# Kernel tuning notes

Measured on AMD Instinct MI355X. Metric: run time of the kernel, lower is better.

The kernel has to match this reference:

```python
import jax, jax.numpy as jnp
import numpy as np

NEG_SLOPE = 0.2

def setup_inputs() -> dict:
    key = jax.random.key(0)
    ks = jax.random.split(key, 10)
    N, E, D = 50000, 1250000, 64
    indices = jax.random.randint(ks[0], (2, E), 0, N, dtype=jnp.int64)
    features = jax.random.normal(ks[1], (N, D), dtype=jnp.float32)
    edge_types = jax.random.randint(ks[2], (E,), 0, 4, dtype=jnp.int64)
    s = 1.0 / np.sqrt(D)
    return {
        "indices": indices,
        "features": features,
        "edge_types": edge_types,
        "num_nodes": N,
        "W1_w": jax.random.uniform(ks[3], (D, D), jnp.float32, -s, s),
        "W1_b": jax.random.uniform(ks[4], (D,), jnp.float32, -s, s),
        "W2_w": jax.random.uniform(ks[5], (D, D), jnp.float32, -s, s),
        "W2_b": jax.random.uniform(ks[6], (D,), jnp.float32, -s, s),
        "W_att_w": jax.random.uniform(ks[7], (D, D), jnp.float32, -s, s),
        "W_att_b": jax.random.uniform(ks[8], (D,), jnp.float32, -s, s),
        "a": jax.random.normal(ks[9], (2 * D, 1), jnp.float32) * np.sqrt(2.0 / (2 * D + 1)),
    }


def reference(indices, features, edge_types, num_nodes, W1_w, W1_b, W2_w, W2_b, W_att_w, W_att_b, a):
    src, dst = indices[0], indices[1]
    D = W_att_w.shape[0]
    scaling = 1.0 / jnp.sqrt(jnp.float32(D))

    # Attention transform; cat([h_src, h_dst]) @ a == h_src@a1 + h_dst@a2
    h_trans = features @ W_att_w.T + W_att_b              # (N, D)
    a1, a2 = a[:D, 0], a[D:, 0]
    s_src = h_trans @ a1                                  # (N,)
    s_dst = h_trans @ a2                                  # (N,)
    e_raw = s_src[src] + s_dst[dst]                       # (E,)

    bias = jnp.where(edge_types == 0, 5.0, 0.0)           # ingredient bias
    e = jax.nn.leaky_relu((e_raw + bias) * scaling, NEG_SLOPE).astype(jnp.float32)

    # segment softmax over destination nodes (max is detached in original)
    max_score = jax.lax.stop_gradient(jax.ops.segment_max(e, dst, num_segments=num_nodes))
    max_score = jnp.where(jnp.isfinite(max_score), max_score, -1e9)
    exp_e = jnp.exp(e - max_score[dst])                   # (E,)
    denom = jax.ops.segment_sum(exp_e, dst, num_segments=num_nodes)
    alpha = exp_e / (denom[dst] + 1e-9)                   # (E,)

    # message passing
    h_msg = features @ W1_w.T + W1_b                      # (N, D)
    weighted = h_msg[src] * alpha[:, None]                # (E, D)
    h_neigh = jax.ops.segment_sum(weighted, dst, num_segments=num_nodes)  # (N, D)

    h_self = features                                     # in_dim == out_dim
    sum_h = h_self + h_neigh
    prod_h = h_self * h_neigh
    h_out = jax.nn.leaky_relu(sum_h + prod_h @ W2_w.T + W2_b, NEG_SLOPE)
    return h_out
```

## Files before the change

### kernel.cpp

```cpp
#include <hip/hip_runtime.h>
#include <math.h>

#define DD 64
#define WSTR 68
#define NEG_SLOPE 0.2f
#define SCALING 0.125f
#define CAP 64

__device__ __forceinline__ float lrelu(float x) { return x >= 0.0f ? x : NEG_SLOPE * x; }

__device__ __forceinline__ unsigned bf16_rne(float f) {
    unsigned u = __float_as_uint(f);
    u += 0x7FFFu + ((u >> 16) & 1u);
    return u >> 16;
}

__device__ __forceinline__ float bfly_sum64(float v) {
    #pragma unroll
    for (int off = 1; off < 64; off <<= 1) v += __shfl_xor(v, off);
    return v;
}

__global__ void k_prep(const float* __restrict__ Watt, const float* __restrict__ Wattb,
                       const float* __restrict__ a, float* __restrict__ v12,
                       float* __restrict__ c12) {
    int k = threadIdx.x;
    float s1 = 0.f, s2 = 0.f;
    for (int d = 0; d < DD; ++d) {
        float w = Watt[d * DD + k];
        s1 = fmaf(w, a[d], s1);
        s2 = fmaf(w, a[DD + d], s2);
    }
    v12[k] = s1;
    v12[DD + k] = s2;
    float b = Wattb[k];
    float p1 = bfly_sum64(b * a[k]);
    float p2 = bfly_sum64(b * a[DD + k]);
    if (k == 0) { c12[0] = p1; c12[1] = p2; }
}

__global__ __launch_bounds__(256) void k_node1(
        const float* __restrict__ feat, const float* __restrict__ W1,
        const float* __restrict__ W1b, const float* __restrict__ v12,
        const float* __restrict__ c12,
        float* __restrict__ s_src, float* __restrict__ s_dst,
        unsigned short* __restrict__ hmsg16, int N) {
    __shared__ float W1p[DD * WSTR];
    __shared__ float fsh[4][4 * DD];
    int t = threadIdx.x;
    for (int i = t; i < DD * DD; i += 256) {
        int d = i >> 6, k = i & 63;
        W1p[d * WSTR + k] = W1[i];
    }
    __syncthreads();
    int lane = t & 63, wslot = t >> 6;
    float c1 = c12[0], c2 = c12[1];
    float v1l = v12[lane], v2l = v12[DD + lane];
    float b = W1b[lane];
    float* fs = fsh[wslot];
    int n0 = (blockIdx.x * 4 + wslot) * 4;
    if (n0 >= N) return;

    float fd[4], p1[4], p2[4];
    #pragma unroll
    for (int i = 0; i < 4; ++i) {
        int n = n0 + i;
        fd[i] = (n < N) ? feat[n * DD + lane] : 0.f;
        fs[i * DD + lane] = fd[i];
        p1[i] = fd[i] * v1l;
        p2[i] = fd[i] * v2l;
    }
    #pragma unroll
    for (int off = 1; off < 64; off <<= 1) {
        #pragma unroll
        for (int i = 0; i < 4; ++i) {
            p1[i] += __shfl_xor(p1[i], off);
            p2[i] += __shfl_xor(p2[i], off);
        }
    }
    float acc[4] = {b, b, b, b};
    const float4* wrow = (const float4*)&W1p[lane * WSTR];
    #pragma unroll
    for (int k4 = 0; k4 < 16; ++k4) {
        float4 w = wrow[k4];
        #pragma unroll
        for (int i = 0; i < 4; ++i) {
            float4 f = *(const float4*)&fs[i * DD + k4 * 4];
            acc[i] = fmaf(f.x, w.x, acc[i]);
            acc[i] = fmaf(f.y, w.y, acc[i]);
            acc[i] = fmaf(f.z, w.z, acc[i]);
            acc[i] = fmaf(f.w, w.w, acc[i]);
        }
    }
    #pragma unroll
    for (int i = 0; i < 4; ++i) {
        int n = n0 + i;
        if (n < N) {
            hmsg16[n * DD + lane] = (unsigned short)bf16_rne(acc[i]);
            if (lane == 0) { s_src[n] = p1[i] + c1; s_dst[n] = p2[i] + c2; }
        }
    }
}

__global__ void k_bucket(const int* __restrict__ src, const int* __restrict__ dst,
                         const int* __restrict__ et,
                         const float* __restrict__ s_src, const float* __restrict__ s_dst,
                         int* __restrict__ cnt, unsigned* __restrict__ wpack, int E) {
    int i = blockIdx.x * blockDim.x + threadIdx.x;
    if (i >= E) return;
    int d = dst[i], s = src[i];
    float e = s_src[s] + s_dst[d] + (et[i] == 0 ? 5.0f : 0.0f);
    float w = __expf(lrelu(e * SCALING));
    int slot = atomicAdd(&cnt[d], 1);
    if (slot > CAP - 1) slot = CAP - 1;
    wpack[(d << 6) + slot] = (bf16_rne(w) << 16) | (unsigned)s;
}

__global__ __launch_bounds__(256) void k_gather(
        const float* __restrict__ feat, const unsigned* __restrict__ hmsg,
        const float* __restrict__ W2, const float* __restrict__ W2b,
        const int* __restrict__ cnt, const unsigned* __restrict__ wpack,
        float* __restrict__ out, int N) {
    __shared__ float W2p[DD * WSTR];
    __shared__ float plds[4][DD];
    int t = threadIdx.x;
    for (int i = t; i < DD * DD; i += 256) {
        int d = i >> 6, k = i & 63;
        W2p[d * WSTR + k] = W2[i];
    }
    __syncthreads();
    int lane = t & 63, wslot = t >> 6;
    int c = lane & 31, h = lane >> 5;
    int n = (blockIdx.x * 256 + t) >> 6;
    if (n >= N) return;
    int m = cnt[n]; if (m > CAP) m = CAP;
    unsigned u = wpack[(n << 6) + lane];
    if (lane >= m) u = 0;

    float ax = 0.f, ay = 0.f, bx = 0.f, by = 0.f, l = 0.f;
    int tt = 0;
    for (; tt + 8 <= m; tt += 8) {
        unsigned e0 = __shfl(u, tt + h);
        unsigned e1 = __shfl(u, tt + 2 + h);
        unsigned e2 = __shfl(u, tt + 4 + h);
        unsigned e3 = __shfl(u, tt + 6 + h);
        unsigned v0 = hmsg[(e0 & 0xFFFFu) * 32 + c];
        unsigned v1 = hmsg[(e1 & 0xFFFFu) * 32 + c];
        unsigned v2 = hmsg[(e2 & 0xFFFFu) * 32 + c];
        unsigned v3 = hmsg[(e3 & 0xFFFFu) * 32 + c];
        float w0 = __uint_as_float(e0 & 0xFFFF0000u);
        float w1 = __uint_as_float(e1 & 0xFFFF0000u);
        float w2 = __uint_as_float(e2 & 0xFFFF0000u);
        float w3 = __uint_as_float(e3 & 0xFFFF0000u);
        ax = fmaf(w0, __uint_as_float(v0 << 16), ax);
        ay = fmaf(w0, __uint_as_float(v0 & 0xFFFF0000u), ay);
        bx = fmaf(w1, __uint_as_float(v1 << 16), bx);
        by = fmaf(w1, __uint_as_float(v1 & 0xFFFF0000u), by);
        ax = fmaf(w2, __uint_as_float(v2 << 16), ax);
        ay = fmaf(w2, __uint_as_float(v2 & 0xFFFF0000u), ay);
        bx = fmaf(w3, __uint_as_float(v3 << 16), bx);
        by = fmaf(w3, __uint_as_float(v3 & 0xFFFF0000u), by);
        l += (w0 + w1) + (w2 + w3);
    }
    for (; tt < m; tt += 2) {
        unsigned e0 = __shfl(u, tt + h);
        unsigned v0 = hmsg[(e0 & 0xFFFFu) * 32 + c];
        float w0 = __uint_as_float(e0 & 0xFFFF0000u);
        ax = fmaf(w0, __uint_as_float(v0 << 16), ax);
        ay = fmaf(w0, __uint_as_float(v0 & 0xFFFF0000u), ay);
        l += w0;
    }
    ax += bx; ay += by;
    ax += __shfl_xor(ax, 32);
    ay += __shfl_xor(ay, 32);
    l  += __shfl_xor(l, 32);
    float inv = 1.f / (l + 1e-9f);

    float* pl = plds[wslot];
    if (h == 0) { pl[2 * c] = ax * inv; pl[2 * c + 1] = ay * inv; }
    float hn = pl[lane];
    float fd = feat[n * DD + lane];
    pl[lane] = fd * hn;
    float acc2 = W2b[lane];
    const float4* wrow = (const float4*)&W2p[lane * WSTR];
    #pragma unroll
    for (int k4 = 0; k4 < 16; ++k4) {
        float4 w = wrow[k4];
        float4 pk = *(const float4*)&pl[k4 * 4];
        acc2 = fmaf(pk.x, w.x, acc2);
        acc2 = fmaf(pk.y, w.y, acc2);
        acc2 = fmaf(pk.z, w.z, acc2);
        acc2 = fmaf(pk.w, w.w, acc2);
    }
    out[n * DD + lane] = lrelu(fd + hn + acc2);
}

extern "C" void kernel_launch(void* const* d_in, const int* in_sizes, int n_in,
                              void* d_out, int out_size, void* d_ws, size_t ws_size,
                              hipStream_t stream) {
    const int*   indices = (const int*)d_in[0];
    const float* feat    = (const float*)d_in[1];
    const int*   etype   = (const int*)d_in[2];
    const float* W1      = (const float*)d_in[4];
    const float* W1b     = (const float*)d_in[5];
    const float* W2      = (const float*)d_in[6];
    const float* W2b     = (const float*)d_in[7];
    const float* Watt    = (const float*)d_in[8];
    const float* Wattb   = (const float*)d_in[9];
    const float* a       = (const float*)d_in[10];

    const int E = in_sizes[2];
    const int N = in_sizes[1] / DD;
    const int* src = indices;
    const int* dst = indices + E;

    float* ws = (float*)d_ws;
    float*    v12   = ws;
    float*    c12   = ws + 128;
    float*    s_src = ws + 192;
    float*    s_dst = s_src + N;
    int*      cnt   = (int*)(s_dst + N);
    unsigned* hmsg  = (unsigned*)(cnt + N);
    unsigned* wpack = hmsg + (size_t)N * 32;

    hipMemsetAsync(cnt, 0, (size_t)N * sizeof(int), stream);
    k_prep<<<1, 64, 0, stream>>>(Watt, Wattb, a, v12, c12);
    k_node1<<<(N + 15) / 16, 256, 0, stream>>>(feat, W1, W1b, v12, c12,
                                               s_src, s_dst, (unsigned short*)hmsg, N);
    k_bucket<<<(E + 255) / 256, 256, 0, stream>>>(src, dst, etype, s_src, s_dst,
                                                  cnt, wpack, E);
    k_gather<<<(N + 3) / 4, 256, 0, stream>>>(feat, hmsg, W2, W2b,
                                              cnt, wpack, (float*)d_out, N);
}
```

Baseline: 249.8 us.

## Apply W1 after aggregation, gather bf16 features, fold prep kernel, persistent gather

Uses linearity to aggregate weighted bf16 raw features per destination and apply W1 once per node afterwards, with the bias scaled by the weight sum. The separate prep kernel is removed: every node1 block recomputes the attention projection vectors itself, and node1 now only converts features to bf16. The gather kernel becomes a persistent grid-stride loop over 1024 blocks, amortising the load of both weight matrices into shared memory. The cost is a second 64x64 matvec per node in the gather and redundant per-block recomputation of the projection vectors.

```diff
diff --git a/kernel.cpp b/kernel.cpp
--- a/kernel.cpp
+++ b/kernel.cpp
@@ -21,43 +21,29 @@
     return v;
 }
 
-__global__ void k_prep(const float* __restrict__ Watt, const float* __restrict__ Wattb,
-                       const float* __restrict__ a, float* __restrict__ v12,
-                       float* __restrict__ c12) {
-    int k = threadIdx.x;
-    float s1 = 0.f, s2 = 0.f;
-    for (int d = 0; d < DD; ++d) {
-        float w = Watt[d * DD + k];
-        s1 = fmaf(w, a[d], s1);
-        s2 = fmaf(w, a[DD + d], s2);
-    }
-    v12[k] = s1;
-    v12[DD + k] = s2;
-    float b = Wattb[k];
-    float p1 = bfly_sum64(b * a[k]);
-    float p2 = bfly_sum64(b * a[DD + k]);
-    if (k == 0) { c12[0] = p1; c12[1] = p2; }
-}
-
 __global__ __launch_bounds__(256) void k_node1(
-        const float* __restrict__ feat, const float* __restrict__ W1,
-        const float* __restrict__ W1b, const float* __restrict__ v12,
-        const float* __restrict__ c12,
+        const float* __restrict__ feat, const float* __restrict__ Watt,
+        const float* __restrict__ Wattb, const float* __restrict__ a,
         float* __restrict__ s_src, float* __restrict__ s_dst,
-        unsigned short* __restrict__ hmsg16, int N) {
-    __shared__ float W1p[DD * WSTR];
-    __shared__ float fsh[4][4 * DD];
+        unsigned* __restrict__ feat16, int N) {
+    __shared__ float v1s[DD], v2s[DD], csh[2];
     int t = threadIdx.x;
-    for (int i = t; i < DD * DD; i += 256) {
-        int d = i >> 6, k = i & 63;
-        W1p[d * WSTR + k] = W1[i];
+    if (t < 64) {
+        float s1 = 0.f, s2 = 0.f;
+        for (int d = 0; d < DD; ++d) {
+            float w = Watt[d * DD + t];
+            s1 = fmaf(w, a[d], s1);
+            s2 = fmaf(w, a[DD + d], s2);
+        }
+        v1s[t] = s1; v2s[t] = s2;
+        float b = Wattb[t];
+        float p1 = bfly_sum64(b * a[t]);
+        float p2 = bfly_sum64(b * a[DD + t]);
+        if (t == 0) { csh[0] = p1; csh[1] = p2; }
     }
     __syncthreads();
     int lane = t & 63, wslot = t >> 6;
-    float c1 = c12[0], c2 = c12[1];
-    float v1l = v12[lane], v2l = v12[DD + lane];
-    float b = W1b[lane];
-    float* fs = fsh[wslot];
+    float v1l = v1s[lane], v2l = v2s[lane], c1 = csh[0], c2 = csh[1];
     int n0 = (blockIdx.x * 4 + wslot) * 4;
     if (n0 >= N) return;
 
@@ -66,7 +52,6 @@
     for (int i = 0; i < 4; ++i) {
         int n = n0 + i;
         fd[i] = (n < N) ? feat[n * DD + lane] : 0.f;
-        fs[i * DD + lane] = fd[i];
         p1[i] = fd[i] * v1l;
         p2[i] = fd[i] * v2l;
     }
@@ -78,25 +63,14 @@
             p2[i] += __shfl_xor(p2[i], off);
         }
     }
-    float acc[4] = {b, b, b, b};
-    const float4* wrow = (const float4*)&W1p[lane * WSTR];
-    #pragma unroll
-    for (int k4 = 0; k4 < 16; ++k4) {
-        float4 w = wrow[k4];
-        #pragma unroll
-        for (int i = 0; i < 4; ++i) {
-            float4 f = *(const float4*)&fs[i * DD + k4 * 4];
-            acc[i] = fmaf(f.x, w.x, acc[i]);
-            acc[i] = fmaf(f.y, w.y, acc[i]);
-            acc[i] = fmaf(f.z, w.z, acc[i]);
-            acc[i] = fmaf(f.w, w.w, acc[i]);
-        }
-    }
     #pragma unroll
     for (int i = 0; i < 4; ++i) {
         int n = n0 + i;
+        unsigned me = bf16_rne(fd[i]);
+        unsigned pair = me | (__shfl_down(me, 1) << 16);
+        unsigned v = __shfl(pair, 2 * lane);
         if (n < N) {
-            hmsg16[n * DD + lane] = (unsigned short)bf16_rne(acc[i]);
+            if (lane < 32) feat16[n * 32 + lane] = v;
             if (lane == 0) { s_src[n] = p1[i] + c1; s_dst[n] = p2[i] + c2; }
         }
     }
@@ -117,82 +91,98 @@
 }
 
 __global__ __launch_bounds__(256) void k_gather(
-        const float* __restrict__ feat, const unsigned* __restrict__ hmsg,
+        const float* __restrict__ feat, const unsigned* __restrict__ feat16,
+        const float* __restrict__ W1, const float* __restrict__ W1b,
         const float* __restrict__ W2, const float* __restrict__ W2b,
         const int* __restrict__ cnt, const unsigned* __restrict__ wpack,
         float* __restrict__ out, int N) {
-    __shared__ float W2p[DD * WSTR];
+    __shared__ float W1p[DD * WSTR], W2p[DD * WSTR];
     __shared__ float plds[4][DD];
     int t = threadIdx.x;
     for (int i = t; i < DD * DD; i += 256) {
         int d = i >> 6, k = i & 63;
+        W1p[d * WSTR + k] = W1[i];
         W2p[d * WSTR + k] = W2[i];
     }
     __syncthreads();
     int lane = t & 63, wslot = t >> 6;
     int c = lane & 31, h = lane >> 5;
-    int n = (blockIdx.x * 256 + t) >> 6;
-    if (n >= N) return;
-    int m = cnt[n]; if (m > CAP) m = CAP;
-    unsigned u = wpack[(n << 6) + lane];
-    if (lane >= m) u = 0;
-
-    float ax = 0.f, ay = 0.f, bx = 0.f, by = 0.f, l = 0.f;
-    int tt = 0;
-    for (; tt + 8 <= m; tt += 8) {
-        unsigned e0 = __shfl(u, tt + h);
-        unsigned e1 = __shfl(u, tt + 2 + h);
-        unsigned e2 = __shfl(u, tt + 4 + h);
-        unsigned e3 = __shfl(u, tt + 6 + h);
-        unsigned v0 = hmsg[(e0 & 0xFFFFu) * 32 + c];
-        unsigned v1 = hmsg[(e1 & 0xFFFFu) * 32 + c];
-        unsigned v2 = hmsg[(e2 & 0xFFFFu) * 32 + c];
-        unsigned v3 = hmsg[(e3 & 0xFFFFu) * 32 + c];
-        float w0 = __uint_as_float(e0 & 0xFFFF0000u);
-        float w1 = __uint_as_float(e1 & 0xFFFF0000u);
-        float w2 = __uint_as_float(e2 & 0xFFFF0000u);
-        float w3 = __uint_as_float(e3 & 0xFFFF0000u);
-        ax = fmaf(w0, __uint_as_float(v0 << 16), ax);
-        ay = fmaf(w0, __uint_as_float(v0 & 0xFFFF0000u), ay);
-        bx = fmaf(w1, __uint_as_float(v1 << 16), bx);
-        by = fmaf(w1, __uint_as_float(v1 & 0xFFFF0000u), by);
-        ax = fmaf(w2, __uint_as_float(v2 << 16), ax);
-        ay = fmaf(w2, __uint_as_float(v2 & 0xFFFF0000u), ay);
-        bx = fmaf(w3, __uint_as_float(v3 << 16), bx);
-        by = fmaf(w3, __uint_as_float(v3 & 0xFFFF0000u), by);
-        l += (w0 + w1) + (w2 + w3);
-    }
-    for (; tt < m; tt += 2) {
-        unsigned e0 = __shfl(u, tt + h);
-        unsigned v0 = hmsg[(e0 & 0xFFFFu) * 32 + c];
-        float w0 = __uint_as_float(e0 & 0xFFFF0000u);
-        ax = fmaf(w0, __uint_as_float(v0 << 16), ax);
-        ay = fmaf(w0, __uint_as_float(v0 & 0xFFFF0000u), ay);
-        l += w0;
-    }
-    ax += bx; ay += by;
-    ax += __shfl_xor(ax, 32);
-    ay += __shfl_xor(ay, 32);
-    l  += __shfl_xor(l, 32);
-    float inv = 1.f / (l + 1e-9f);
-
+    float b1l = W1b[lane], b2l = W2b[lane];
+    const float4* wrow1 = (const float4*)&W1p[lane * WSTR];
+    const float4* wrow2 = (const float4*)&W2p[lane * WSTR];
     float* pl = plds[wslot];
-    if (h == 0) { pl[2 * c] = ax * inv; pl[2 * c + 1] = ay * inv; }
-    float hn = pl[lane];
-    float fd = feat[n * DD + lane];
-    pl[lane] = fd * hn;
-    float acc2 = W2b[lane];
-    const float4* wrow = (const float4*)&W2p[lane * WSTR];
-    #pragma unroll
-    for (int k4 = 0; k4 < 16; ++k4) {
-        float4 w = wrow[k4];
-        float4 pk = *(const float4*)&pl[k4 * 4];
-        acc2 = fmaf(pk.x, w.x, acc2);
-        acc2 = fmaf(pk.y, w.y, acc2);
-        acc2 = fmaf(pk.z, w.z, acc2);
-        acc2 = fmaf(pk.w, w.w, acc2);
-    }
-    out[n * DD + lane] = lrelu(fd + hn + acc2);
+    int wv = blockIdx.x * 4 + wslot;
+    int nw = gridDim.x * 4;
+    for (int n = wv; n < N; n += nw) {
+        int m = cnt[n]; if (m > CAP) m = CAP;
+        unsigned u = wpack[(n << 6) + lane];
+        if (lane >= m) u = 0;
+
+        float ax = 0.f, ay = 0.f, bx = 0.f, by = 0.f, l = 0.f;
+        int tt = 0;
+        for (; tt + 8 <= m; tt += 8) {
+            unsigned e0 = __shfl(u, tt + h);
+            unsigned e1 = __shfl(u, tt + 2 + h);
+            unsigned e2 = __shfl(u, tt + 4 + h);
+            unsigned e3 = __shfl(u, tt + 6 + h);
+            unsigned v0 = feat16[(e0 & 0xFFFFu) * 32 + c];
+            unsigned v1 = feat16[(e1 & 0xFFFFu) * 32 + c];
+            unsigned v2 = feat16[(e2 & 0xFFFFu) * 32 + c];
+            unsigned v3 = feat16[(e3 & 0xFFFFu) * 32 + c];
+            float w0 = __uint_as_float(e0 & 0xFFFF0000u);
+            float w1 = __uint_as_float(e1 & 0xFFFF0000u);
+            float w2 = __uint_as_float(e2 & 0xFFFF0000u);
+            float w3 = __uint_as_float(e3 & 0xFFFF0000u);
+            ax = fmaf(w0, __uint_as_float(v0 << 16), ax);
+            ay = fmaf(w0, __uint_as_float(v0 & 0xFFFF0000u), ay);
+            bx = fmaf(w1, __uint_as_float(v1 << 16), bx);
+            by = fmaf(w1, __uint_as_float(v1 & 0xFFFF0000u), by);
+            ax = fmaf(w2, __uint_as_float(v2 << 16), ax);
+            ay = fmaf(w2, __uint_as_float(v2 & 0xFFFF0000u), ay);
+            bx = fmaf(w3, __uint_as_float(v3 << 16), bx);
+            by = fmaf(w3, __uint_as_float(v3 & 0xFFFF0000u), by);
+            l += (w0 + w1) + (w2 + w3);
+        }
+        for (; tt < m; tt += 2) {
+            unsigned e0 = __shfl(u, tt + h);
+            unsigned v0 = feat16[(e0 & 0xFFFFu) * 32 + c];
+            float w0 = __uint_as_float(e0 & 0xFFFF0000u);
+            ax = fmaf(w0, __uint_as_float(v0 << 16), ax);
+            ay = fmaf(w0, __uint_as_float(v0 & 0xFFFF0000u), ay);
+            l += w0;
+        }
+        ax += bx; ay += by;
+        ax += __shfl_xor(ax, 32);
+        ay += __shfl_xor(ay, 32);
+        l  += __shfl_xor(l, 32);
+        float inv = 1.f / (l + 1e-9f);
+
+        if (h == 0) { pl[2 * c] = ax; pl[2 * c + 1] = ay; }
+        float acc1 = l * b1l;
+        #pragma unroll
+        for (int k4 = 0; k4 < 16; ++k4) {
+            float4 w = wrow1[k4];
+            float4 g = *(const float4*)&pl[k4 * 4];
+            acc1 = fmaf(g.x, w.x, acc1);
+            acc1 = fmaf(g.y, w.y, acc1);
+            acc1 = fmaf(g.z, w.z, acc1);
+            acc1 = fmaf(g.w, w.w, acc1);
+        }
+        float hn = acc1 * inv;
+        float fd = feat[n * DD + lane];
+        pl[lane] = fd * hn;
+        float acc2 = b2l;
+        #pragma unroll
+        for (int k4 = 0; k4 < 16; ++k4) {
+            float4 w = wrow2[k4];
+            float4 pk = *(const float4*)&pl[k4 * 4];
+            acc2 = fmaf(pk.x, w.x, acc2);
+            acc2 = fmaf(pk.y, w.y, acc2);
+            acc2 = fmaf(pk.z, w.z, acc2);
+            acc2 = fmaf(pk.w, w.w, acc2);
+        }
+        out[n * DD + lane] = lrelu(fd + hn + acc2);
+    }
 }
 
 extern "C" void kernel_launch(void* const* d_in, const int* in_sizes, int n_in,
@@ -215,20 +205,17 @@
     const int* dst = indices + E;
 
     float* ws = (float*)d_ws;
-    float*    v12   = ws;
-    float*    c12   = ws + 128;
-    float*    s_src = ws + 192;
-    float*    s_dst = s_src + N;
-    int*      cnt   = (int*)(s_dst + N);
-    unsigned* hmsg  = (unsigned*)(cnt + N);
-    unsigned* wpack = hmsg + (size_t)N * 32;
+    float*    s_src  = ws;
+    float*    s_dst  = s_src + N;
+    int*      cnt    = (int*)(s_dst + N);
+    unsigned* feat16 = (unsigned*)(cnt + N);
+    unsigned* wpack  = feat16 + (size_t)N * 32;
 
     hipMemsetAsync(cnt, 0, (size_t)N * sizeof(int), stream);
-    k_prep<<<1, 64, 0, stream>>>(Watt, Wattb, a, v12, c12);
-    k_node1<<<(N + 15) / 16, 256, 0, stream>>>(feat, W1, W1b, v12, c12,
-                                               s_src, s_dst, (unsigned short*)hmsg, N);
+    k_node1<<<(N + 15) / 16, 256, 0, stream>>>(feat, Watt, Wattb, a,
+                                               s_src, s_dst, feat16, N);
     k_bucket<<<(E + 255) / 256, 256, 0, stream>>>(src, dst, etype, s_src, s_dst,
                                                   cnt, wpack, E);
-    k_gather<<<(N + 3) / 4, 256, 0, stream>>>(feat, hmsg, W2, W2b,
-                                              cnt, wpack, (float*)d_out, N);
-}
+    k_gather<<<1024, 256, 0, stream>>>(feat, feat16, W1, W1b, W2, W2b,
+                                       cnt, wpack, (float*)d_out, N);
+}
```

Result: faster. 205.3 us (-17.8%).
